# Kernel optimization log

Measured on AMD Instinct MI355X. Metric: run time of the kernel, lower is better.

## Reference

```python
import jax, jax.numpy as jnp
import numpy as np

N = 16384; E = 262144; B = 8
IN = 768; HID = 256; H1 = 4; OUT = 128; H2 = 2

def setup_inputs() -> dict:
    key = jax.random.key(0)
    ks = jax.random.split(key, 16)
    s = 0.02
    def p(k, shape):
        return jax.random.normal(k, shape, jnp.float32) * s
    return {
        "x": jax.random.normal(ks[0], (N, IN), jnp.float32),
        "edge_index": jax.random.randint(ks[1], (2, E), 0, N),
        "batch": jnp.sort(jax.random.randint(ks[2], (N,), 0, B)),
        "W1": p(ks[3], (H1 * HID, IN)),
        "a_src1": p(ks[4], (H1, HID)),
        "a_dst1": p(ks[5], (H1, HID)),
        "b1": jnp.zeros((H1 * HID,), jnp.float32),
        "W2": p(ks[6], (H2 * OUT, H1 * HID)),
        "a_src2": p(ks[7], (H2, OUT)),
        "a_dst2": p(ks[8], (H2, OUT)),
        "b2": jnp.zeros((OUT,), jnp.float32),
        "proj_W": p(ks[9], (768, OUT)),
        "proj_b": jnp.zeros((768,), jnp.float32),
        "ln_g": jnp.ones((768,), jnp.float32),
        "ln_b": jnp.zeros((768,), jnp.float32),
        "rh_W1": p(ks[10], (32, OUT + 2)),
        "rh_b1": jnp.zeros((32,), jnp.float32),
        "rh_W2": p(ks[11], (1, 32)),
        "rh_b2": jnp.zeros((1,), jnp.float32),
        "num_graphs": B,
    }

def _gat(x, src, dst, W, a_s, a_d, bias, heads, ch, concat, n):
    # PyG GATConv (shared src/dst lin): h = x W^T -> [n, heads, ch]
    h = (x @ W.T).reshape(n, heads, ch)
    al_s = (h * a_s).sum(-1)  # [n, heads]
    al_d = (h * a_d).sum(-1)
    e = jax.nn.leaky_relu(al_s[src] + al_d[dst], 0.2)  # [E', heads]
    # segment softmax over incoming edges of each destination node
    m = jax.lax.stop_gradient(jax.ops.segment_max(e, dst, num_segments=n))
    ex = jnp.exp(e - m[dst])
    den = jax.ops.segment_sum(ex, dst, num_segments=n)
    w = ex / (den[dst] + 1e-16)
    out = jax.ops.segment_sum(w[:, :, None] * h[src], dst, num_segments=n)
    if concat:
        return out.reshape(n, heads * ch) + bias
    return out.mean(1) + bias

def reference(x, edge_index, batch, W1, a_src1, a_dst1, b1, W2, a_src2, a_dst2, b2,
              proj_W, proj_b, ln_g, ln_b, rh_W1, rh_b1, rh_W2, rh_b2, num_graphs):
    n = x.shape[0]
    src0, dst0 = edge_index[0], edge_index[1]
    loop = jnp.arange(n)  # GATConv adds self-loops by default
    src = jnp.concatenate([src0, loop])
    dst = jnp.concatenate([dst0, loop])
    h1 = jax.nn.elu(_gat(x, src, dst, W1, a_src1, a_dst1, b1, H1, HID, True, n))
    h2 = jax.nn.elu(_gat(h1, src, dst, W2, a_src2, a_dst2, b2, H2, OUT, False, n))
    # global mean pool per graph
    n_g = jax.ops.segment_sum(jnp.ones((n,), x.dtype), batch, num_segments=num_graphs)
    pooled = jax.ops.segment_sum(h2, batch, num_segments=num_graphs) / jnp.maximum(n_g, 1.0)[:, None]
    pe = pooled @ proj_W.T + proj_b
    mu = pe.mean(-1, keepdims=True)
    var = pe.var(-1, keepdims=True)
    struct_embed = (pe - mu) / jnp.sqrt(var + 1e-5) * ln_g + ln_b
    # topology stats from ORIGINAL edges (no self-loops), per original code
    e_g = jax.ops.segment_sum(jnp.ones((src0.shape[0],), x.dtype), batch[src0], num_segments=num_graphs)
    stats = jnp.stack([e_g / (n_g + 1e-6), jnp.log(n_g + 1.0)], axis=-1)  # [B, 2]
    ri = jnp.concatenate([pooled, stats], axis=-1)
    hid = jax.nn.relu(ri @ rh_W1.T + rh_b1)
    prop_risk = jax.nn.sigmoid(hid @ rh_W2.T + rh_b2)[:, 0]
    return struct_embed, h2, prop_risk
```

## Files before the change

### kernel.cpp

```cpp
#include <hip/hip_runtime.h>
#include <math.h>

#define NN    16384
#define EE    262144
#define ET    (EE + NN)
#define NB    8
#define IN_F  768
#define HID1  256
#define H1    4
#define D1    (H1*HID1)
#define OUT2  128
#define H2    2
#define D2    (H2*OUT2)

typedef __attribute__((ext_vector_type(8))) short short8;
typedef __attribute__((ext_vector_type(4))) float f32x4;

__device__ __forceinline__ unsigned short f2bf(float v) {
    unsigned u = __float_as_uint(v);
    u = (u + 0x7FFFu + ((u >> 16) & 1u)) >> 16;
    return (unsigned short)u;
}
__device__ __forceinline__ float bf2f(unsigned short b) {
    return __uint_as_float((unsigned)b << 16);
}


__global__ void hist_kernel(const int* __restrict__ ei, const int* __restrict__ batch,
                            int* __restrict__ deg, int* __restrict__ n_g, int* __restrict__ e_cnt) {
    __shared__ int le[NB], ln[NB];
    int tid = threadIdx.x;
    if (tid < NB) { le[tid] = 0; ln[tid] = 0; }
    __syncthreads();
    int t = blockIdx.x * blockDim.x + tid;
    if (t < EE) {
        int s = ei[t];
        int d = ei[EE + t];
        atomicAdd(&deg[d], 1);
        atomicAdd(&le[batch[s]], 1);
    }
    if (t < NN) {
        atomicAdd(&ln[batch[t]], 1);
    }
    __syncthreads();
    if (tid < NB) {
        if (le[tid]) atomicAdd(&e_cnt[tid], le[tid]);
        if (ln[tid]) atomicAdd(&n_g[tid], ln[tid]);
    }
}

__global__ __launch_bounds__(1024) void scan_kernel(const int* __restrict__ deg, int* __restrict__ row_ptr) {
    __shared__ int sums[1024];
    int t = threadIdx.x;
    int base = t * 16;
    int local[16];
    int acc = 0;
#pragma unroll
    for (int i = 0; i < 16; i++) { local[i] = acc; acc += deg[base + i] + 1; }
    sums[t] = acc;
    __syncthreads();
    for (int off = 1; off < 1024; off <<= 1) {
        int v = (t >= off) ? sums[t - off] : 0;
        __syncthreads();
        sums[t] += v;
        __syncthreads();
    }
    int prev = (t == 0) ? 0 : sums[t - 1];
#pragma unroll
    for (int i = 0; i < 16; i++) row_ptr[base + i] = prev + local[i];
    if (t == 1023) row_ptr[NN] = sums[1023];
}

__global__ void scatter_kernel(const int* __restrict__ ei, const int* __restrict__ row_ptr,
                               int* __restrict__ cursor, int* __restrict__ colidx) {
    int t = blockIdx.x * blockDim.x + threadIdx.x;
    if (t >= ET) return;
    int s, d;
    if (t < EE) { s = ei[t]; d = ei[EE + t]; }
    else        { s = d = t - EE; }
    int pos = row_ptr[d] + atomicAdd(&cursor[d], 1);
    colidx[pos] = s;
}


__global__ void split_kernel(const float* __restrict__ in, unsigned short* __restrict__ hi,
                             unsigned short* __restrict__ lo, int n4) {
    int i = blockIdx.x * blockDim.x + threadIdx.x;
    if (i >= n4) return;
    float4 v = ((const float4*)in)[i];
    ushort4 h, l;
    h.x = f2bf(v.x); l.x = f2bf(v.x - bf2f(h.x));
    h.y = f2bf(v.y); l.y = f2bf(v.y - bf2f(h.y));
    h.z = f2bf(v.z); l.z = f2bf(v.z - bf2f(h.z));
    h.w = f2bf(v.w); l.w = f2bf(v.w - bf2f(h.w));
    ((ushort4*)hi)[i] = h;
    ((ushort4*)lo)[i] = l;
}

__global__ void tobf_kernel(const float* __restrict__ in, unsigned short* __restrict__ hi, int n4) {
    int i = blockIdx.x * blockDim.x + threadIdx.x;
    if (i >= n4) return;
    float4 v = ((const float4*)in)[i];
    ushort4 h;
    h.x = f2bf(v.x); h.y = f2bf(v.y); h.z = f2bf(v.z); h.w = f2bf(v.w);
    ((ushort4*)hi)[i] = h;
}


__device__ __forceinline__ void ld_lds16(const unsigned short* g, unsigned short* l) {
    __builtin_amdgcn_global_load_lds((__attribute__((address_space(1))) void*)g,
                                     (__attribute__((address_space(3))) void*)l, 16, 0, 0);
}

#define BM 128
#define BN 128
#define BK 32

template <int TERMS>
__global__ __launch_bounds__(256) void gemm_mfma(const unsigned short* __restrict__ Ahi,
                                                 const unsigned short* __restrict__ Alo,
                                                 const unsigned short* __restrict__ Bhi,
                                                 const unsigned short* __restrict__ Blo,
                                                 unsigned short* __restrict__ Cb,
                                                 int M, int N, int K) {
    __shared__ __align__(16) unsigned short sA[2][BM * BK];
    __shared__ __align__(16) unsigned short sB[2][BN * BK];
    int t = threadIdx.x;
    int lane = t & 63, wave = t >> 6;

    int NC = N / BN;
    int b = blockIdx.x;
    int xcd = b & 7;
    int idx = b >> 3;
    int c = idx % NC;
    int rg = idx / NC;
    int bm = (rg * 8 + xcd) * BM;
    int bn = c * BN;

    int wm = (wave & 1) * 64, wn = (wave >> 1) * 64;

    const unsigned short* gbase;
    unsigned short* lbase;
    if      (wave == 0) { gbase = Ahi + (size_t)bm * K; lbase = sA[0]; }
    else if (wave == 1) { gbase = Alo + (size_t)bm * K; lbase = sA[1]; }
    else if (wave == 2) { gbase = Bhi + (size_t)bn * K; lbase = sB[0]; }
    else                { gbase = (TERMS == 3 ? Blo : Bhi) + (size_t)bn * K; lbase = sB[1]; }
    bool do_stage = (wave < 3) || (TERMS == 3);
    int schunk = (lane & 3) ^ ((lane >> 3) & 3);
    const unsigned short* gsrc = gbase + (size_t)(lane >> 2) * K + schunk * 8;

    f32x4 zero = {0.f, 0.f, 0.f, 0.f};
    f32x4 acc[4][4];
#pragma unroll
    for (int i = 0; i < 4; i++)
#pragma unroll
        for (int j = 0; j < 4; j++) acc[i][j] = zero;

    int row16 = lane & 15;
    int kq = ((lane >> 4) ^ ((row16 >> 1) & 3)) * 8;

    for (int k0 = 0; k0 < K; k0 += BK) {
        if (do_stage) {
#pragma unroll
            for (int i = 0; i < 8; i++)
                ld_lds16(gsrc + k0 + (size_t)(i * 16) * K, lbase + i * 16 * BK);
        }
        __syncthreads();

        short8 ah[4], alo[4], bh[4], blo[4];
#pragma unroll
        for (int mt = 0; mt < 4; mt++) {
            int r = (wm + mt * 16 + row16) * BK + kq;
            ah[mt]  = *(const short8*)&sA[0][r];
            alo[mt] = *(const short8*)&sA[1][r];
        }
#pragma unroll
        for (int nt = 0; nt < 4; nt++) {
            int r = (wn + nt * 16 + row16) * BK + kq;
            bh[nt]  = *(const short8*)&sB[0][r];
            if (TERMS == 3) blo[nt] = *(const short8*)&sB[1][r];
        }
#pragma unroll
        for (int mt = 0; mt < 4; mt++)
#pragma unroll
            for (int nt = 0; nt < 4; nt++) {
                acc[mt][nt] = __builtin_amdgcn_mfma_f32_16x16x32_bf16(ah[mt],  bh[nt],  acc[mt][nt], 0, 0, 0);
                acc[mt][nt] = __builtin_amdgcn_mfma_f32_16x16x32_bf16(alo[mt], bh[nt],  acc[mt][nt], 0, 0, 0);
                if (TERMS == 3)
                    acc[mt][nt] = __builtin_amdgcn_mfma_f32_16x16x32_bf16(ah[mt], blo[nt], acc[mt][nt], 0, 0, 0);
            }
        __syncthreads();
    }

    int crow0 = bm + wm + (lane >> 4) * 4;
    int ccol0 = bn + wn + row16;
#pragma unroll
    for (int mt = 0; mt < 4; mt++)
#pragma unroll
        for (int nt = 0; nt < 4; nt++)
#pragma unroll
            for (int reg = 0; reg < 4; reg++)
                Cb[(size_t)(crow0 + mt * 16 + reg) * N + ccol0 + nt * 16] = f2bf(acc[mt][nt][reg]);
}


template <int H, int CH>
__global__ void al_kernel(const unsigned short* __restrict__ h, const float* __restrict__ a_s,
                          const float* __restrict__ a_d, float* __restrict__ als,
                          float* __restrict__ ald) {
    int node = blockIdx.x;
    int wave = threadIdx.x >> 6;
    int lane = threadIdx.x & 63;
    const unsigned short* row = h + (size_t)node * (H * CH) + wave * CH;
    float ss = 0.f, sd = 0.f;
#pragma unroll
    for (int c = lane; c < CH; c += 64) {
        float v = bf2f(row[c]);
        ss += v * a_s[wave * CH + c];
        sd += v * a_d[wave * CH + c];
    }
#pragma unroll
    for (int off = 32; off; off >>= 1) {
        ss += __shfl_down(ss, off);
        sd += __shfl_down(sd, off);
    }
    if (lane == 0) {
        als[node * H + wave] = ss;
        ald[node * H + wave] = sd;
    }
}

__device__ __forceinline__ float leaky(float v) { return v > 0.f ? v : 0.2f * v; }
__device__ __forceinline__ float elu1(float v) { return v > 0.f ? v : (__expf(v) - 1.f); }


__global__ __launch_bounds__(256) void agg1_kernel(const unsigned short* __restrict__ h,
                                                   const float* __restrict__ als,
                                                   const float* __restrict__ ald,
                                                   const int* __restrict__ row_ptr,
                                                   const int* __restrict__ colidx,
                                                   const float* __restrict__ bias,
                                                   unsigned short* __restrict__ out_hi,
                                                   unsigned short* __restrict__ out_lo) {
    int b = blockIdx.x;
    int s = b & 7;
    int g = b >> 3;
    int wave = threadIdx.x >> 6;
    int lane = threadIdx.x & 63;
    int lanesel = lane & 32;
    int l5 = lane & 31;
    int d = g * 8 + wave * 2 + (lanesel >> 5);
    int head = s >> 1;
    int start = row_ptr[d], end = row_ptr[d + 1];
    int deg = end - start;
    int degO = __shfl_xor(deg, 32);
    int degmax = max(deg, degO);
    float ald_h = ald[d * H1 + head];
    unsigned choff = (unsigned)(s * 128 + l5 * 4);

    float a0 = 0.f, a1 = 0.f, a2 = 0.f, a3 = 0.f;
    float wsum = 0.f;

    for (int c0 = 0; c0 < degmax; c0 += 32) {
        int ee = start + c0 + l5;
        int idx = ee < end ? ee : end - 1;
        int sL = colidx[idx];
        float ev = leaky(als[(sL << 2) + head] + ald_h);
        float wL = (ee < end) ? __expf(ev) : 0.f;
        float ws = wL;
        ws += __shfl_xor(ws, 16); ws += __shfl_xor(ws, 8);
        ws += __shfl_xor(ws, 4);  ws += __shfl_xor(ws, 2);  ws += __shfl_xor(ws, 1);
        wsum += ws;

        int n = degmax - c0; if (n > 32) n = 32;
        int n8 = (n + 7) & ~7;
        for (int k = 0; k < n8; k += 8) {
            ushort4 hv[8]; float wv[8];
#pragma unroll
            for (int j = 0; j < 8; j++) {
                int src = k + j + lanesel;
                int ssj = __shfl(sL, src);
                wv[j]   = __shfl(wL, src);
                hv[j] = *(const ushort4*)(h + (((unsigned)ssj << 10) + choff));
            }
#pragma unroll
            for (int j = 0; j < 8; j++) {
                float w = wv[j];
                a0 += w * bf2f(hv[j].x); a1 += w * bf2f(hv[j].y);
                a2 += w * bf2f(hv[j].z); a3 += w * bf2f(hv[j].w);
            }
        }
    }

    float sinv = 1.f / (wsum + 1e-16f);
    float4 bv = *(const float4*)(bias + s * 128 + l5 * 4);
    float o0 = elu1(a0 * sinv + bv.x);
    float o1 = elu1(a1 * sinv + bv.y);
    float o2 = elu1(a2 * sinv + bv.z);
    float o3 = elu1(a3 * sinv + bv.w);
    ushort4 oh, ol;
    oh.x = f2bf(o0); ol.x = f2bf(o0 - bf2f(oh.x));
    oh.y = f2bf(o1); ol.y = f2bf(o1 - bf2f(oh.y));
    oh.z = f2bf(o2); ol.z = f2bf(o2 - bf2f(oh.z));
    oh.w = f2bf(o3); ol.w = f2bf(o3 - bf2f(oh.w));
    size_t o = (size_t)d * D1 + choff;
    *(ushort4*)(out_hi + o) = oh;
    *(ushort4*)(out_lo + o) = ol;
}


__global__ __launch_bounds__(256) void agg2_kernel(const unsigned short* __restrict__ h,
                                                   const float* __restrict__ als,
                                                   const float* __restrict__ ald,
                                                   const int* __restrict__ row_ptr,
                                                   const int* __restrict__ colidx,
                                                   const float* __restrict__ bias,
                                                   float* __restrict__ out) {
    int wave = threadIdx.x >> 6;
    int lane = threadIdx.x & 63;
    int lanesel = lane & 32;
    int l5 = lane & 31;
    int head = lanesel >> 5;
    int d = blockIdx.x * 4 + wave;
    int start = row_ptr[d], end = row_ptr[d + 1];
    int deg = end - start;
    float ald_h = ald[d * H2 + head];
    unsigned ch4 = (unsigned)(lane << 2);

    float a0 = 0.f, a1 = 0.f, a2 = 0.f, a3 = 0.f;
    float wsum = 0.f;

    for (int c0 = 0; c0 < deg; c0 += 32) {
        int ee = start + c0 + l5;
        int idx = ee < end ? ee : end - 1;
        int sL = colidx[idx];
        float ev = leaky(als[(sL << 1) + head] + ald_h);
        float wL = (ee < end) ? __expf(ev) : 0.f;
        float ws = wL;
        ws += __shfl_xor(ws, 16); ws += __shfl_xor(ws, 8);
        ws += __shfl_xor(ws, 4);  ws += __shfl_xor(ws, 2);  ws += __shfl_xor(ws, 1);
        wsum += ws;

        int n = deg - c0; if (n > 32) n = 32;
        int n8 = (n + 7) & ~7;
        for (int k = 0; k < n8; k += 8) {
            ushort4 hv[8]; float wv[8];
#pragma unroll
            for (int j = 0; j < 8; j++) {
                int ssj = __builtin_amdgcn_readlane(sL, k + j);
                wv[j] = __shfl(wL, k + j + lanesel);
                hv[j] = *(const ushort4*)(h + (((unsigned)ssj << 8) + ch4));
            }
#pragma unroll
            for (int j = 0; j < 8; j++) {
                float w = wv[j];
                a0 += w * bf2f(hv[j].x); a1 += w * bf2f(hv[j].y);
                a2 += w * bf2f(hv[j].z); a3 += w * bf2f(hv[j].w);
            }
        }
    }

    float sinv = 1.f / (wsum + 1e-16f);
    float r0 = a0 * sinv, r1 = a1 * sinv, r2 = a2 * sinv, r3 = a3 * sinv;
    r0 += __shfl_xor(r0, 32);
    r1 += __shfl_xor(r1, 32);
    r2 += __shfl_xor(r2, 32);
    r3 += __shfl_xor(r3, 32);
    if (lane < 32) {
        float4 bv = *(const float4*)(bias + (l5 << 2));
        float4 o;
        o.x = elu1(r0 * 0.5f + bv.x);
        o.y = elu1(r1 * 0.5f + bv.y);
        o.z = elu1(r2 * 0.5f + bv.z);
        o.w = elu1(r3 * 0.5f + bv.w);
        *(float4*)(out + (size_t)d * OUT2 + (l5 << 2)) = o;
    }
}


__global__ __launch_bounds__(256) void pool_kernel(const float* __restrict__ h2,
                                                   const int* __restrict__ batch,
                                                   float* __restrict__ pooled) {
    int c = threadIdx.x & 127;
    int half = threadIdx.x >> 7;
    int n0 = blockIdx.x * 256 + half;
    int nend = blockIdx.x * 256 + 256;
    float acc = 0.f;
    int curg = batch[n0];
    for (int n = n0; n < nend; n += 2) {
        int g = batch[n];
        if (g != curg) {
            atomicAdd(&pooled[curg * OUT2 + c], acc);
            acc = 0.f; curg = g;
        }
        acc += h2[(size_t)n * OUT2 + c];
    }
    atomicAdd(&pooled[curg * OUT2 + c], acc);
}


__global__ __launch_bounds__(256) void final_kernel(const float* __restrict__ pooled_sum,
                                                    const int* __restrict__ n_g_i,
                                                    const int* __restrict__ e_cnt,
                                                    const float* __restrict__ projW,
                                                    const float* __restrict__ projb,
                                                    const float* __restrict__ lng,
                                                    const float* __restrict__ lnb,
                                                    const float* __restrict__ rhW1,
                                                    const float* __restrict__ rhb1,
                                                    const float* __restrict__ rhW2,
                                                    const float* __restrict__ rhb2,
                                                    float* __restrict__ out_se,
                                                    float* __restrict__ out_risk) {
    int b = blockIdx.x;
    int t = threadIdx.x;
    __shared__ float pooled[OUT2];
    __shared__ float pe[768];
    __shared__ float red[256];
    __shared__ float hid[32];
    __shared__ float stat_mu, stat_inv;

    float ng = (float)n_g_i[b];
    if (t < OUT2) pooled[t] = pooled_sum[b * OUT2 + t] / fmaxf(ng, 1.0f);
    __syncthreads();

    for (int j = t; j < 768; j += 256) {
        const float* wr = projW + (size_t)j * OUT2;
        float s = projb[j];
        for (int c = 0; c < OUT2; c++) s += pooled[c] * wr[c];
        pe[j] = s;
    }
    __syncthreads();

    float ls = 0.f, lq = 0.f;
    for (int j = t; j < 768; j += 256) { float v = pe[j]; ls += v; lq += v * v; }
    red[t] = ls;
    __syncthreads();
    for (int off = 128; off; off >>= 1) { if (t < off) red[t] += red[t + off]; __syncthreads(); }
    float tot = red[0];
    __syncthreads();
    red[t] = lq;
    __syncthreads();
    for (int off = 128; off; off >>= 1) { if (t < off) red[t] += red[t + off]; __syncthreads(); }
    float totq = red[0];
    if (t == 0) {
        float mu = tot / 768.f;
        float var = totq / 768.f - mu * mu;
        stat_mu = mu;
        stat_inv = 1.f / sqrtf(var + 1e-5f);
    }
    __syncthreads();
    float mu = stat_mu, inv = stat_inv;
    for (int j = t; j < 768; j += 256)
        out_se[(size_t)b * 768 + j] = (pe[j] - mu) * inv * lng[j] + lnb[j];

    float s0 = (float)e_cnt[b] / (ng + 1e-6f);
    float s1 = logf(ng + 1.0f);
    if (t < 32) {
        const float* wr = rhW1 + t * (OUT2 + 2);
        float s = rhb1[t];
        for (int c = 0; c < OUT2; c++) s += pooled[c] * wr[c];
        s += s0 * wr[OUT2] + s1 * wr[OUT2 + 1];
        hid[t] = fmaxf(s, 0.f);
    }
    __syncthreads();
    if (t == 0) {
        float s = rhb2[0];
        for (int k = 0; k < 32; k++) s += hid[k] * rhW2[k];
        out_risk[b] = 1.f / (1.f + __expf(-s));
    }
}


extern "C" void kernel_launch(void* const* d_in, const int* in_sizes, int n_in,
                              void* d_out, int out_size, void* d_ws, size_t ws_size,
                              hipStream_t stream) {
    const float* x     = (const float*)d_in[0];
    const int*   ei    = (const int*)  d_in[1];
    const int*   batch = (const int*)  d_in[2];
    const float* W1    = (const float*)d_in[3];
    const float* a_s1  = (const float*)d_in[4];
    const float* a_d1  = (const float*)d_in[5];
    const float* b1    = (const float*)d_in[6];
    const float* W2    = (const float*)d_in[7];
    const float* a_s2  = (const float*)d_in[8];
    const float* a_d2  = (const float*)d_in[9];
    const float* b2    = (const float*)d_in[10];
    const float* projW = (const float*)d_in[11];
    const float* projb = (const float*)d_in[12];
    const float* lng   = (const float*)d_in[13];
    const float* lnb   = (const float*)d_in[14];
    const float* rhW1  = (const float*)d_in[15];
    const float* rhb1  = (const float*)d_in[16];
    const float* rhW2  = (const float*)d_in[17];
    const float* rhb2  = (const float*)d_in[18];

    char* ws = (char*)d_ws;
    size_t off = 0;
    auto alloc = [&](size_t bytes) -> void* {
        void* p = ws + off;
        off += (bytes + 255) & ~(size_t)255;
        return p;
    };

    unsigned short* regionA = (unsigned short*)alloc((size_t)2 * NN * D1 * 2);
    unsigned short* x_hi = regionA;
    unsigned short* x_lo = regionA + (size_t)NN * IN_F;
    unsigned short* h1hi = regionA;
    unsigned short* h1lo = regionA + (size_t)NN * D1;

    unsigned short* h1bf = (unsigned short*)alloc((size_t)NN * D1 * 2);
    unsigned short* h2bf = (unsigned short*)alloc((size_t)NN * D2 * 2);
    unsigned short* W1hi = (unsigned short*)alloc((size_t)D1 * IN_F * 2);
    unsigned short* W2hi = (unsigned short*)alloc((size_t)D2 * D1 * 2);
    unsigned short* W2lo = (unsigned short*)alloc((size_t)D2 * D1 * 2);
    float* als1   = (float*)alloc((size_t)NN * H1 * 4);
    float* ald1   = (float*)alloc((size_t)NN * H1 * 4);
    float* als2   = (float*)alloc((size_t)NN * H2 * 4);
    float* ald2   = (float*)alloc((size_t)NN * H2 * 4);
    int*   row_ptr= (int*)  alloc((size_t)(NN + 1) * 4);
    int*   colidx = (int*)  alloc((size_t)ET * 4);
    size_t zoff = off;
    int*   deg    = (int*)  alloc((size_t)NN * 4);
    int*   cursor = (int*)  alloc((size_t)NN * 4);
    int*   n_g    = (int*)  alloc((size_t)NB * 4);
    int*   e_cnt  = (int*)  alloc((size_t)NB * 4);
    float* pooled = (float*)alloc((size_t)NB * OUT2 * 4);
    size_t zbytes = off - zoff;

    float* out_se   = (float*)d_out;
    float* h2out    = out_se + NB * 768;
    float* out_risk = h2out + (size_t)NN * OUT2;

    hipMemsetAsync(ws + zoff, 0, zbytes, stream);

    hist_kernel<<<(EE + 255) / 256, 256, 0, stream>>>(ei, batch, deg, n_g, e_cnt);
    scan_kernel<<<1, 1024, 0, stream>>>(deg, row_ptr);
    scatter_kernel<<<(ET + 255) / 256, 256, 0, stream>>>(ei, row_ptr, cursor, colidx);

    split_kernel<<<((NN * IN_F / 4) + 255) / 256, 256, 0, stream>>>(x, x_hi, x_lo, NN * IN_F / 4);
    tobf_kernel<<<((D1 * IN_F / 4) + 255) / 256, 256, 0, stream>>>(W1, W1hi, D1 * IN_F / 4);
    split_kernel<<<((D2 * D1 / 4) + 255) / 256, 256, 0, stream>>>(W2, W2hi, W2lo, D2 * D1 / 4);

    gemm_mfma<2><<<(NN / BM) * (D1 / BN), 256, 0, stream>>>(x_hi, x_lo, W1hi, W1hi, h1bf, NN, D1, IN_F);
    al_kernel<H1, HID1><<<NN, H1 * 64, 0, stream>>>(h1bf, a_s1, a_d1, als1, ald1);
    agg1_kernel<<<NN, 256, 0, stream>>>(h1bf, als1, ald1, row_ptr, colidx, b1, h1hi, h1lo);

    gemm_mfma<3><<<(NN / BM) * (D2 / BN), 256, 0, stream>>>(h1hi, h1lo, W2hi, W2lo, h2bf, NN, D2, D1);
    al_kernel<H2, OUT2><<<NN, H2 * 64, 0, stream>>>(h2bf, a_s2, a_d2, als2, ald2);
    agg2_kernel<<<NN / 4, 256, 0, stream>>>(h2bf, als2, ald2, row_ptr, colidx, b2, h2out);

    pool_kernel<<<NN / 256, 256, 0, stream>>>(h2out, batch, pooled);

    final_kernel<<<NB, 256, 0, stream>>>(pooled, n_g, e_cnt, projW, projb, lng, lnb,
                                         rhW1, rhb1, rhW2, rhb2, out_se, out_risk);
}
```

Baseline: 444.7 us.

## Switch GEMMs from split-bf16 multi-term MFMA to single-term fp16 MFMA

Replaces the hi/lo bf16 split scheme (2 or 3 MFMA terms per tile) with a single fp16 conversion of inputs, weights and intermediates, feeding one f16 MFMA per tile. This removes the extra MFMA work, halves staging traffic and LDS use, and drops the lo-buffer writes from the split kernels and from the layer-1 aggregation, which now uses a nontemporal packed store. The trade-off is lower precision: fp16 has a narrower range and keeps about 11 mantissa bits, so there is some risk to accuracy tolerance and to overflow on larger activations.

```diff
diff --git a/kernel.cpp b/kernel.cpp
--- a/kernel.cpp
+++ b/kernel.cpp
@@ -13,16 +13,14 @@
 #define H2    2
 #define D2    (H2*OUT2)
 
-typedef __attribute__((ext_vector_type(8))) short short8;
+typedef __attribute__((ext_vector_type(8))) _Float16 f16x8;
 typedef __attribute__((ext_vector_type(4))) float f32x4;
 
-__device__ __forceinline__ unsigned short f2bf(float v) {
-    unsigned u = __float_as_uint(v);
-    u = (u + 0x7FFFu + ((u >> 16) & 1u)) >> 16;
-    return (unsigned short)u;
-}
-__device__ __forceinline__ float bf2f(unsigned short b) {
-    return __uint_as_float((unsigned)b << 16);
+__device__ __forceinline__ float hf2f(unsigned short u) {
+    union { unsigned short u; _Float16 h; } c; c.u = u; return (float)c.h;
+}
+__device__ __forceinline__ unsigned short f2hf(float f) {
+    union { unsigned short u; _Float16 h; } c; c.h = (_Float16)f; return c.u;
 }
 
 
@@ -83,27 +81,13 @@
 }
 
 
-__global__ void split_kernel(const float* __restrict__ in, unsigned short* __restrict__ hi,
-                             unsigned short* __restrict__ lo, int n4) {
-    int i = blockIdx.x * blockDim.x + threadIdx.x;
-    if (i >= n4) return;
-    float4 v = ((const float4*)in)[i];
-    ushort4 h, l;
-    h.x = f2bf(v.x); l.x = f2bf(v.x - bf2f(h.x));
-    h.y = f2bf(v.y); l.y = f2bf(v.y - bf2f(h.y));
-    h.z = f2bf(v.z); l.z = f2bf(v.z - bf2f(h.z));
-    h.w = f2bf(v.w); l.w = f2bf(v.w - bf2f(h.w));
-    ((ushort4*)hi)[i] = h;
-    ((ushort4*)lo)[i] = l;
-}
-
-__global__ void tobf_kernel(const float* __restrict__ in, unsigned short* __restrict__ hi, int n4) {
+__global__ void tohalf_kernel(const float* __restrict__ in, unsigned short* __restrict__ o, int n4) {
     int i = blockIdx.x * blockDim.x + threadIdx.x;
     if (i >= n4) return;
     float4 v = ((const float4*)in)[i];
     ushort4 h;
-    h.x = f2bf(v.x); h.y = f2bf(v.y); h.z = f2bf(v.z); h.w = f2bf(v.w);
-    ((ushort4*)hi)[i] = h;
+    h.x = f2hf(v.x); h.y = f2hf(v.y); h.z = f2hf(v.z); h.w = f2hf(v.w);
+    ((ushort4*)o)[i] = h;
 }
 
 
@@ -116,15 +100,12 @@
 #define BN 128
 #define BK 32
 
-template <int TERMS>
-__global__ __launch_bounds__(256) void gemm_mfma(const unsigned short* __restrict__ Ahi,
-                                                 const unsigned short* __restrict__ Alo,
-                                                 const unsigned short* __restrict__ Bhi,
-                                                 const unsigned short* __restrict__ Blo,
-                                                 unsigned short* __restrict__ Cb,
+__global__ __launch_bounds__(256) void gemm_mfma(const unsigned short* __restrict__ A,
+                                                 const unsigned short* __restrict__ B,
+                                                 unsigned short* __restrict__ C,
                                                  int M, int N, int K) {
-    __shared__ __align__(16) unsigned short sA[2][BM * BK];
-    __shared__ __align__(16) unsigned short sB[2][BN * BK];
+    __shared__ __align__(16) unsigned short sA[BM * BK];
+    __shared__ __align__(16) unsigned short sB[BN * BK];
     int t = threadIdx.x;
     int lane = t & 63, wave = t >> 6;
 
@@ -141,11 +122,11 @@
 
     const unsigned short* gbase;
     unsigned short* lbase;
-    if      (wave == 0) { gbase = Ahi + (size_t)bm * K; lbase = sA[0]; }
-    else if (wave == 1) { gbase = Alo + (size_t)bm * K; lbase = sA[1]; }
-    else if (wave == 2) { gbase = Bhi + (size_t)bn * K; lbase = sB[0]; }
-    else                { gbase = (TERMS == 3 ? Blo : Bhi) + (size_t)bn * K; lbase = sB[1]; }
-    bool do_stage = (wave < 3) || (TERMS == 3);
+    {
+        int hrow = (wave & 1) * 64;
+        if (wave < 2) { gbase = A + (size_t)(bm + hrow) * K; lbase = sA + hrow * BK; }
+        else          { gbase = B + (size_t)(bn + hrow) * K; lbase = sB + hrow * BK; }
+    }
     int schunk = (lane & 3) ^ ((lane >> 3) & 3);
     const unsigned short* gsrc = gbase + (size_t)(lane >> 2) * K + schunk * 8;
 
@@ -160,35 +141,23 @@
     int kq = ((lane >> 4) ^ ((row16 >> 1) & 3)) * 8;
 
     for (int k0 = 0; k0 < K; k0 += BK) {
-        if (do_stage) {
-#pragma unroll
-            for (int i = 0; i < 8; i++)
-                ld_lds16(gsrc + k0 + (size_t)(i * 16) * K, lbase + i * 16 * BK);
-        }
+#pragma unroll
+        for (int i = 0; i < 4; i++)
+            ld_lds16(gsrc + k0 + (size_t)(i * 16) * K, lbase + i * 16 * BK);
         __syncthreads();
 
-        short8 ah[4], alo[4], bh[4], blo[4];
-#pragma unroll
-        for (int mt = 0; mt < 4; mt++) {
-            int r = (wm + mt * 16 + row16) * BK + kq;
-            ah[mt]  = *(const short8*)&sA[0][r];
-            alo[mt] = *(const short8*)&sA[1][r];
-        }
-#pragma unroll
-        for (int nt = 0; nt < 4; nt++) {
-            int r = (wn + nt * 16 + row16) * BK + kq;
-            bh[nt]  = *(const short8*)&sB[0][r];
-            if (TERMS == 3) blo[nt] = *(const short8*)&sB[1][r];
-        }
+        f16x8 ah[4], bh[4];
 #pragma unroll
         for (int mt = 0; mt < 4; mt++)
-#pragma unroll
-            for (int nt = 0; nt < 4; nt++) {
-                acc[mt][nt] = __builtin_amdgcn_mfma_f32_16x16x32_bf16(ah[mt],  bh[nt],  acc[mt][nt], 0, 0, 0);
-                acc[mt][nt] = __builtin_amdgcn_mfma_f32_16x16x32_bf16(alo[mt], bh[nt],  acc[mt][nt], 0, 0, 0);
-                if (TERMS == 3)
-                    acc[mt][nt] = __builtin_amdgcn_mfma_f32_16x16x32_bf16(ah[mt], blo[nt], acc[mt][nt], 0, 0, 0);
-            }
+            ah[mt] = *(const f16x8*)&sA[(wm + mt * 16 + row16) * BK + kq];
+#pragma unroll
+        for (int nt = 0; nt < 4; nt++)
+            bh[nt] = *(const f16x8*)&sB[(wn + nt * 16 + row16) * BK + kq];
+#pragma unroll
+        for (int mt = 0; mt < 4; mt++)
+#pragma unroll
+            for (int nt = 0; nt < 4; nt++)
+                acc[mt][nt] = __builtin_amdgcn_mfma_f32_16x16x32_f16(ah[mt], bh[nt], acc[mt][nt], 0, 0, 0);
         __syncthreads();
     }
 
@@ -200,7 +169,7 @@
         for (int nt = 0; nt < 4; nt++)
 #pragma unroll
             for (int reg = 0; reg < 4; reg++)
-                Cb[(size_t)(crow0 + mt * 16 + reg) * N + ccol0 + nt * 16] = f2bf(acc[mt][nt][reg]);
+                C[(size_t)(crow0 + mt * 16 + reg) * N + ccol0 + nt * 16] = f2hf(acc[mt][nt][reg]);
 }
 
 
@@ -215,7 +184,7 @@
     float ss = 0.f, sd = 0.f;
 #pragma unroll
     for (int c = lane; c < CH; c += 64) {
-        float v = bf2f(row[c]);
+        float v = hf2f(row[c]);
         ss += v * a_s[wave * CH + c];
         sd += v * a_d[wave * CH + c];
     }
@@ -240,8 +209,7 @@
                                                    const int* __restrict__ row_ptr,
                                                    const int* __restrict__ colidx,
                                                    const float* __restrict__ bias,
-                                                   unsigned short* __restrict__ out_hi,
-                                                   unsigned short* __restrict__ out_lo) {
+                                                   unsigned short* __restrict__ outp) {
     int b = blockIdx.x;
     int s = b & 7;
     int g = b >> 3;
@@ -286,8 +254,8 @@
 #pragma unroll
             for (int j = 0; j < 8; j++) {
                 float w = wv[j];
-                a0 += w * bf2f(hv[j].x); a1 += w * bf2f(hv[j].y);
-                a2 += w * bf2f(hv[j].z); a3 += w * bf2f(hv[j].w);
+                a0 += w * hf2f(hv[j].x); a1 += w * hf2f(hv[j].y);
+                a2 += w * hf2f(hv[j].z); a3 += w * hf2f(hv[j].w);
             }
         }
     }
@@ -298,14 +266,12 @@
     float o1 = elu1(a1 * sinv + bv.y);
     float o2 = elu1(a2 * sinv + bv.z);
     float o3 = elu1(a3 * sinv + bv.w);
-    ushort4 oh, ol;
-    oh.x = f2bf(o0); ol.x = f2bf(o0 - bf2f(oh.x));
-    oh.y = f2bf(o1); ol.y = f2bf(o1 - bf2f(oh.y));
-    oh.z = f2bf(o2); ol.z = f2bf(o2 - bf2f(oh.z));
-    oh.w = f2bf(o3); ol.w = f2bf(o3 - bf2f(oh.w));
+    unsigned long long pk = (unsigned long long)f2hf(o0)
+                          | ((unsigned long long)f2hf(o1) << 16)
+                          | ((unsigned long long)f2hf(o2) << 32)
+                          | ((unsigned long long)f2hf(o3) << 48);
     size_t o = (size_t)d * D1 + choff;
-    *(ushort4*)(out_hi + o) = oh;
-    *(ushort4*)(out_lo + o) = ol;
+    __builtin_nontemporal_store(pk, (unsigned long long*)(outp + o));
 }
 
 
@@ -354,8 +320,8 @@
 #pragma unroll
             for (int j = 0; j < 8; j++) {
                 float w = wv[j];
-                a0 += w * bf2f(hv[j].x); a1 += w * bf2f(hv[j].y);
-                a2 += w * bf2f(hv[j].z); a3 += w * bf2f(hv[j].w);
+                a0 += w * hf2f(hv[j].x); a1 += w * hf2f(hv[j].y);
+                a2 += w * hf2f(hv[j].z); a3 += w * hf2f(hv[j].w);
             }
         }
     }
@@ -503,17 +469,14 @@
         return p;
     };
 
-    unsigned short* regionA = (unsigned short*)alloc((size_t)2 * NN * D1 * 2);
-    unsigned short* x_hi = regionA;
-    unsigned short* x_lo = regionA + (size_t)NN * IN_F;
-    unsigned short* h1hi = regionA;
-    unsigned short* h1lo = regionA + (size_t)NN * D1;
-
-    unsigned short* h1bf = (unsigned short*)alloc((size_t)NN * D1 * 2);
-    unsigned short* h2bf = (unsigned short*)alloc((size_t)NN * D2 * 2);
-    unsigned short* W1hi = (unsigned short*)alloc((size_t)D1 * IN_F * 2);
-    unsigned short* W2hi = (unsigned short*)alloc((size_t)D2 * D1 * 2);
-    unsigned short* W2lo = (unsigned short*)alloc((size_t)D2 * D1 * 2);
+    unsigned short* regionA = (unsigned short*)alloc((size_t)NN * D1 * 2);
+    unsigned short* x_f  = regionA;
+    unsigned short* h1a  = regionA;
+
+    unsigned short* h1f  = (unsigned short*)alloc((size_t)NN * D1 * 2);
+    unsigned short* h2ft = (unsigned short*)alloc((size_t)NN * D2 * 2);
+    unsigned short* W1f  = (unsigned short*)alloc((size_t)D1 * IN_F * 2);
+    unsigned short* W2f  = (unsigned short*)alloc((size_t)D2 * D1 * 2);
     float* als1   = (float*)alloc((size_t)NN * H1 * 4);
     float* ald1   = (float*)alloc((size_t)NN * H1 * 4);
     float* als2   = (float*)alloc((size_t)NN * H2 * 4);
@@ -538,17 +501,17 @@
     scan_kernel<<<1, 1024, 0, stream>>>(deg, row_ptr);
     scatter_kernel<<<(ET + 255) / 256, 256, 0, stream>>>(ei, row_ptr, cursor, colidx);
 
-    split_kernel<<<((NN * IN_F / 4) + 255) / 256, 256, 0, stream>>>(x, x_hi, x_lo, NN * IN_F / 4);
-    tobf_kernel<<<((D1 * IN_F / 4) + 255) / 256, 256, 0, stream>>>(W1, W1hi, D1 * IN_F / 4);
-    split_kernel<<<((D2 * D1 / 4) + 255) / 256, 256, 0, stream>>>(W2, W2hi, W2lo, D2 * D1 / 4);
-
-    gemm_mfma<2><<<(NN / BM) * (D1 / BN), 256, 0, stream>>>(x_hi, x_lo, W1hi, W1hi, h1bf, NN, D1, IN_F);
-    al_kernel<H1, HID1><<<NN, H1 * 64, 0, stream>>>(h1bf, a_s1, a_d1, als1, ald1);
-    agg1_kernel<<<NN, 256, 0, stream>>>(h1bf, als1, ald1, row_ptr, colidx, b1, h1hi, h1lo);
-
-    gemm_mfma<3><<<(NN / BM) * (D2 / BN), 256, 0, stream>>>(h1hi, h1lo, W2hi, W2lo, h2bf, NN, D2, D1);
-    al_kernel<H2, OUT2><<<NN, H2 * 64, 0, stream>>>(h2bf, a_s2, a_d2, als2, ald2);
-    agg2_kernel<<<NN / 4, 256, 0, stream>>>(h2bf, als2, ald2, row_ptr, colidx, b2, h2out);
+    tohalf_kernel<<<((NN * IN_F / 4) + 255) / 256, 256, 0, stream>>>(x, x_f, NN * IN_F / 4);
+    tohalf_kernel<<<((D1 * IN_F / 4) + 255) / 256, 256, 0, stream>>>(W1, W1f, D1 * IN_F / 4);
+    tohalf_kernel<<<((D2 * D1 / 4) + 255) / 256, 256, 0, stream>>>(W2, W2f, D2 * D1 / 4);
+
+    gemm_mfma<<<(NN / BM) * (D1 / BN), 256, 0, stream>>>(x_f, W1f, h1f, NN, D1, IN_F);
+    al_kernel<H1, HID1><<<NN, H1 * 64, 0, stream>>>(h1f, a_s1, a_d1, als1, ald1);
+    agg1_kernel<<<NN, 256, 0, stream>>>(h1f, als1, ald1, row_ptr, colidx, b1, h1a);
+
+    gemm_mfma<<<(NN / BM) * (D2 / BN), 256, 0, stream>>>(h1a, W2f, h2ft, NN, D2, D1);
+    al_kernel<H2, OUT2><<<NN, H2 * 64, 0, stream>>>(h2ft, a_s2, a_d2, als2, ald2);
+    agg2_kernel<<<NN / 4, 256, 0, stream>>>(h2ft, als2, ald2, row_ptr, colidx, b2, h2out);
 
     pool_kernel<<<NN / 256, 256, 0, stream>>>(h2out, batch, pooled);
 
```

After: 406.0 us. 8.7% less time.
